# Performance work log

Measured on AMD Instinct MI355X. Metric: run time of the kernel, lower is better.

Reference implementation:

```python
import jax, jax.numpy as jnp
import numpy as np

B, S, T, H, E, V, PAD = 128, 400, 50, 512, 128, 50000, 1000


def setup_inputs() -> dict:
    key = jax.random.key(0)
    ks = jax.random.split(key, 20)
    inp = {
        "input_token": jax.random.randint(ks[0], (B, 1), 0, V),
        "prev_decoder_h_states": jax.random.normal(ks[1], (B, T, H), jnp.float32),
        "last_hidden": jax.random.normal(ks[2], (B, H), jnp.float32),
        "encoder_states": jax.random.normal(ks[3], (B, S, H), jnp.float32),
        "full_input_var": jax.random.randint(ks[4], (B, S), 0, V + PAD),
        "previous_att": jax.random.normal(ks[5], (B, T, S), jnp.float32),
        "control_var": jax.random.normal(ks[6], (B, 1), jnp.float32),
        # learned parameters
        "emb": jax.random.normal(ks[7], (V, E), jnp.float32) * 0.02,
        "W_ih": jax.random.normal(ks[8], (3 * H, E), jnp.float32) * 0.05,
        "W_hh": jax.random.normal(ks[9], (3 * H, H), jnp.float32) * 0.05,
        "b_ih": jnp.zeros((3 * H,), jnp.float32),
        "b_hh": jnp.zeros((3 * H,), jnp.float32),
        "w_h": jax.random.normal(ks[10], (H,), jnp.float32) * 0.05,
        "w_d": jax.random.normal(ks[11], (H,), jnp.float32) * 0.05,
        "gen_W": jax.random.normal(ks[12], (1, 3 * H + 1), jnp.float32) * 0.05,
        "gen_b": jnp.zeros((1,), jnp.float32),
        "outh_W": jax.random.normal(ks[13], (E, 3 * H + 1), jnp.float32) * 0.05,
        "outh_b": jnp.zeros((E,), jnp.float32),
        "outv_W": jax.random.normal(ks[14], (V, E), jnp.float32) * 0.02,
        "outv_b": jnp.zeros((V,), jnp.float32),
    }
    return inp


def reference(input_token, prev_decoder_h_states, last_hidden, encoder_states,
              full_input_var, previous_att, control_var,
              emb, W_ih, W_hh, b_ih, b_hh, w_h, w_d,
              gen_W, gen_b, outh_W, outh_b, outv_W, outv_b):
    # embedding lookup (dropout = eval-mode identity); seq len is 1
    x = emb[input_token[:, 0]]                              # [B,E]
    # single GRU step (torch gate order: r, z, n)
    gx = x @ W_ih.T + b_ih                                  # [B,3H]
    gh = last_hidden @ W_hh.T + b_hh                        # [B,3H]
    r = jax.nn.sigmoid(gx[:, :H] + gh[:, :H])
    z = jax.nn.sigmoid(gx[:, H:2 * H] + gh[:, H:2 * H])
    n = jnp.tanh(gx[:, 2 * H:] + r * gh[:, 2 * H:])
    h = (1.0 - z) * n + z * last_hidden                     # decoder_hidden [B,H]

    # temporal encoder attention (previous_att is not None branch)
    att_scores = jnp.einsum("bh,bsh->bs", h, w_h[None, None, :] * encoder_states)
    temporal = jnp.exp(att_scores) / jnp.exp(previous_att).sum(1)   # [B,S]
    new_previous_att = jnp.concatenate([previous_att, att_scores[:, None, :]], axis=1)
    att_dist = temporal / temporal.sum(-1, keepdims=True)           # [B,S]

    # intra-decoder attention
    dec_scores = jnp.einsum("bh,bth->bt", h, w_d[None, None, :] * prev_decoder_h_states)
    dec_att = jax.nn.softmax(dec_scores, axis=-1)                   # [B,T]
    decoder_context = jnp.einsum("bt,bth->bh", dec_att, prev_decoder_h_states)

    encoder_context = jnp.einsum("bs,bsh->bh", att_dist, encoder_states)
    combined = jnp.concatenate([h, encoder_context, decoder_context, control_var], axis=-1)  # [B,3H+1]

    p_vocab = jax.nn.softmax((combined @ outh_W.T + outh_b) @ outv_W.T + outv_b, axis=-1)    # [B,V]
    p_gen = jax.nn.sigmoid(combined @ gen_W.T + gen_b)                                       # [B,1]

    # copy distribution via scatter-add over extended vocab V+PAD
    token_input_dist = jnp.zeros((input_token.shape[0], V + PAD), p_vocab.dtype)
    rows = jnp.arange(input_token.shape[0])[:, None]
    token_input_dist = token_input_dist.at[rows, full_input_var].add(att_dist)

    p_final = jnp.pad(p_vocab * p_gen, ((0, 0), (0, PAD))) + (1.0 - p_gen) * token_input_dist
    decoder_h_states = jnp.concatenate([prev_decoder_h_states, h[:, None, :]], axis=1)
    return (p_final, p_gen, p_vocab, att_dist, decoder_h_states, h, new_previous_att)
```

## Files before the change

### kernel.cpp

```cpp
#include <hip/hip_runtime.h>
#include <hip/hip_bf16.h>
#include <math.h>

constexpr int B = 128, S = 400, T = 50, H = 512, E = 128, V = 50000, PADV = 1000;
constexpr int NV = V + PADV;
constexpr int TH1 = 3 * H + 1;

constexpr int O_PFINAL = 0;
constexpr int O_PGEN   = O_PFINAL + B * NV;
constexpr int O_PVOCAB = O_PGEN + B;
constexpr int O_ATT    = O_PVOCAB + B * V;
constexpr int O_DHS    = O_ATT + B * S;
constexpr int O_H      = O_DHS + B * (T + 1) * H;
constexpr int O_NPA    = O_H + B * H;

constexpr int W_X    = 0;
constexpr int W_GX   = W_X + B * E;
constexpr int W_GH   = W_GX + B * 3 * H;
constexpr int W_HW   = W_GH + B * 3 * H;
constexpr int W_HD   = W_HW + B * H;
constexpr int W_SC   = W_HD + B * H;
constexpr int W_DEN  = W_SC + B * S;
constexpr int W_CMB  = W_DEN + B * S;
constexpr int W_LE   = W_CMB + B * TH1;
constexpr int W_RMAX = W_LE + B * E;
constexpr int W_RSUM = W_RMAX + B;
constexpr int W_PM   = W_RSUM + B;
constexpr int W_PS   = W_PM + B * 10;

__device__ __forceinline__ float wave_sum(float v) {
#pragma unroll
  for (int o = 32; o > 0; o >>= 1) v += __shfl_xor(v, o);
  return v;
}

__global__ void k_init(const int* __restrict__ tok, const float* __restrict__ emb,
                       const float* __restrict__ ctrl, float* __restrict__ ws) {
  int i = blockIdx.x * 256 + threadIdx.x;
  if (i < B * E) {
    int b = i >> 7, e = i & 127;
    ws[W_X + i] = emb[tok[b] * E + e];
  }
  if (i < B * H) {
    int b = i >> 9, h = i & 511;
    ws[W_CMB + b * TH1 + H + h] = 0.f;
  }
  if (i < B) ws[W_CMB + i * TH1 + 3 * H] = ctrl[i];
#pragma unroll
  for (int j = 0; j < 3; ++j) ws[W_GH + i + j * 65536] = 0.f;
}

__global__ __launch_bounds__(256) void k_grugemm(
    const float* __restrict__ x, const float* __restrict__ lh,
    const float* __restrict__ Wih, const float* __restrict__ Whh,
    float* __restrict__ ws) {
  __shared__ float As[32][132];
  __shared__ float Ws[32][36];
  const int tid = threadIdx.x;
  const int n0 = blockIdx.x * 32;
  const int y = blockIdx.y;
  const bool g0 = (y == 0);
  const float* A = g0 ? x : lh;
  const float* W = g0 ? Wih : Whh;
  const int K = g0 ? E : H;
  const int kbase = g0 ? 0 : (y - 1) * 128;
  const int tc = tid & 15;
  const int tr = tid >> 4;
  float acc[8][2] = {};
  for (int c = 0; c < 4; ++c) {
    const int k0 = kbase + c * 32;
    {
      int i = tid;
#pragma unroll
      for (int it = 0; it < 4; ++it, i += 256) {
        int b = i >> 3, k4 = i & 7;
        float4 v = *(const float4*)&A[b * K + k0 + k4 * 4];
        As[k4 * 4 + 0][b] = v.x; As[k4 * 4 + 1][b] = v.y;
        As[k4 * 4 + 2][b] = v.z; As[k4 * 4 + 3][b] = v.w;
      }
    }
    {
      int n = tid >> 3, k4 = tid & 7;
      float4 v = *(const float4*)&W[(n0 + n) * K + k0 + k4 * 4];
      Ws[k4 * 4 + 0][n] = v.x; Ws[k4 * 4 + 1][n] = v.y;
      Ws[k4 * 4 + 2][n] = v.z; Ws[k4 * 4 + 3][n] = v.w;
    }
    __syncthreads();
#pragma unroll
    for (int kk = 0; kk < 32; ++kk) {
      float4 a0 = *(const float4*)&As[kk][tr * 8];
      float4 a1 = *(const float4*)&As[kk][tr * 8 + 4];
      float2 w = *(const float2*)&Ws[kk][tc * 2];
      float av[8] = {a0.x, a0.y, a0.z, a0.w, a1.x, a1.y, a1.z, a1.w};
#pragma unroll
      for (int i = 0; i < 8; ++i) {
        acc[i][0] += av[i] * w.x;
        acc[i][1] += av[i] * w.y;
      }
    }
    __syncthreads();
  }
  if (g0) {
#pragma unroll
    for (int i = 0; i < 8; ++i) {
      float* dst = ws + W_GX + (tr * 8 + i) * (3 * H) + n0 + tc * 2;
      dst[0] = acc[i][0]; dst[1] = acc[i][1];
    }
  } else {
#pragma unroll
    for (int i = 0; i < 8; ++i) {
      float* dst = ws + W_GH + (tr * 8 + i) * (3 * H) + n0 + tc * 2;
      atomicAdd(dst, acc[i][0]); atomicAdd(dst + 1, acc[i][1]);
    }
  }
}

__global__ void k_gates(const float* __restrict__ ws_in, const float* __restrict__ lh,
                        const float* __restrict__ bih, const float* __restrict__ bhh,
                        const float* __restrict__ w_h, const float* __restrict__ w_d,
                        float* __restrict__ ws, float* __restrict__ out) {
  int i = blockIdx.x * 256 + threadIdx.x;
  int b = i >> 9, u = i & 511;
  const float* gx = ws_in + W_GX + b * (3 * H);
  const float* gh = ws_in + W_GH + b * (3 * H);
  float gxr = gx[u] + bih[u], gxz = gx[H + u] + bih[H + u], gxn = gx[2 * H + u] + bih[2 * H + u];
  float ghr = gh[u] + bhh[u], ghz = gh[H + u] + bhh[H + u], ghn = gh[2 * H + u] + bhh[2 * H + u];
  float r = 1.f / (1.f + __expf(-(gxr + ghr)));
  float z = 1.f / (1.f + __expf(-(gxz + ghz)));
  float n = tanhf(gxn + r * ghn);
  float lhv = lh[i];
  float h = (1.f - z) * n + z * lhv;
  out[O_H + i] = h;
  out[O_DHS + b * ((T + 1) * H) + T * H + u] = h;
  ws[W_CMB + b * TH1 + u] = h;
  ws[W_HW + i] = h * w_h[u];
  ws[W_HD + i] = h * w_d[u];
}

__global__ void k_den(const float* __restrict__ pa, float* __restrict__ ws,
                      float* __restrict__ out) {
  int i = blockIdx.x * 256 + threadIdx.x;
  if (i >= B * S) return;
  int b = i / S, s = i - b * S;
  float acc = 0.f;
  for (int t = 0; t < T; ++t) {
    float v = pa[(b * T + t) * S + s];
    out[O_NPA + (b * (T + 1) + t) * S + s] = v;
    acc += __expf(v);
  }
  ws[W_DEN + i] = acc;
}

__global__ void k_escore(const float* __restrict__ enc, float* __restrict__ ws,
                         float* __restrict__ out) {
  int blk = blockIdx.x;
  int b = blk / 25, sgrp = blk % 25;
  int wave = threadIdx.x >> 6, lane = threadIdx.x & 63;
  const float4* hw4 = (const float4*)(ws + W_HW + b * H);
  float4 h0 = hw4[lane * 2], h1 = hw4[lane * 2 + 1];
#pragma unroll
  for (int ii = 0; ii < 4; ++ii) {
    int s = sgrp * 16 + wave * 4 + ii;
    const float4* e4 = (const float4*)(enc + (b * S + s) * H);
    float4 e0 = e4[lane * 2], e1 = e4[lane * 2 + 1];
    float d = h0.x * e0.x + h0.y * e0.y + h0.z * e0.z + h0.w * e0.w +
              h1.x * e1.x + h1.y * e1.y + h1.z * e1.z + h1.w * e1.w;
    d = wave_sum(d);
    if (lane == 0) {
      ws[W_SC + b * S + s] = d;
      out[O_NPA + (b * (T + 1) + T) * S + s] = d;
    }
  }
}

__global__ void k_attdist(const float* __restrict__ ws, float* __restrict__ out) {
  int b = blockIdx.x, tid = threadIdx.x;
  __shared__ float red[4];
  int s0 = tid, s1 = tid + 256;
  float t0 = __expf(ws[W_SC + b * S + s0]) / ws[W_DEN + b * S + s0];
  float t1 = 0.f;
  if (s1 < S) t1 = __expf(ws[W_SC + b * S + s1]) / ws[W_DEN + b * S + s1];
  float loc = wave_sum(t0 + t1);
  if ((tid & 63) == 0) red[tid >> 6] = loc;
  __syncthreads();
  float inv = 1.f / (red[0] + red[1] + red[2] + red[3]);
  out[O_ATT + b * S + s0] = t0 * inv;
  if (s1 < S) out[O_ATT + b * S + s1] = t1 * inv;
}

__global__ void k_dec(const float* __restrict__ pd, float* __restrict__ ws,
                      float* __restrict__ out) {
  int b = blockIdx.x, tid = threadIdx.x;
  int wave = tid >> 6, lane = tid & 63;
  __shared__ float sc[T];
  const float4* hd4 = (const float4*)(ws + W_HD + b * H);
  float4 d0 = hd4[lane * 2], d1 = hd4[lane * 2 + 1];
  for (int t = wave; t < T; t += 4) {
    const float4* p4 = (const float4*)(pd + (b * T + t) * H);
    float4 p0 = p4[lane * 2], p1 = p4[lane * 2 + 1];
    float v = d0.x * p0.x + d0.y * p0.y + d0.z * p0.z + d0.w * p0.w +
              d1.x * p1.x + d1.y * p1.y + d1.z * p1.z + d1.w * p1.w;
    v = wave_sum(v);
    if (lane == 0) sc[t] = v;
  }
  __syncthreads();
  if (tid < 64) {
    float v = (lane < T) ? sc[lane] : -1e30f;
    float m = v;
#pragma unroll
    for (int o = 32; o > 0; o >>= 1) m = fmaxf(m, __shfl_xor(m, o));
    float e = (lane < T) ? __expf(v - m) : 0.f;
    float ssum = wave_sum(e);
    if (lane < T) sc[lane] = e / ssum;
  }
  __syncthreads();
  float a0 = 0.f, a1 = 0.f;
  int h0 = tid, h1 = tid + 256;
  for (int t = 0; t < T; ++t) {
    float wt = sc[t];
    a0 += wt * pd[(b * T + t) * H + h0];
    a1 += wt * pd[(b * T + t) * H + h1];
  }
  ws[W_CMB + b * TH1 + 2 * H + h0] = a0;
  ws[W_CMB + b * TH1 + 2 * H + h1] = a1;
  const float4* src = (const float4*)(pd + b * T * H);
  float4* dst = (float4*)(out + O_DHS + b * (T + 1) * H);
  for (int i = tid; i < T * H / 4; i += 256) dst[i] = src[i];
}

__global__ void k_encctx(const float* __restrict__ enc, const float* __restrict__ out,
                         float* __restrict__ ws) {
  int blk = blockIdx.x;
  int b = blk / 5, c = blk % 5;
  int s0 = c * 80, tid = threadIdx.x;
  __shared__ float ad[80];
  if (tid < 80) ad[tid] = out[O_ATT + b * S + s0 + tid];
  __syncthreads();
  float a0 = 0.f, a1 = 0.f;
  int h0 = tid, h1 = tid + 256;
  for (int j = 0; j < 80; ++j) {
    float w = ad[j];
    const float* ep = enc + (b * S + s0 + j) * H;
    a0 += w * ep[h0];
    a1 += w * ep[h1];
  }
  atomicAdd(&ws[W_CMB + b * TH1 + H + h0], a0);
  atomicAdd(&ws[W_CMB + b * TH1 + H + h1], a1);
}

__global__ __launch_bounds__(256) void k_outh2(const float* __restrict__ oW,
                                               const float* __restrict__ ob,
                                               float* __restrict__ ws) {
  __shared__ float cmb[8 * TH1];
  const int tid = threadIdx.x;
  const int b0 = blockIdx.y * 8;
  const int e = blockIdx.x * 4 + (tid >> 6);
  const int lane = tid & 63;
  const float* src = ws + W_CMB + b0 * TH1;
  for (int i = tid; i < 8 * TH1; i += 256) cmb[i] = src[i];
  float wr[25];
  const float* wrow = oW + e * TH1;
#pragma unroll
  for (int j = 0; j < 25; ++j) {
    int k = lane + 64 * j;
    wr[j] = (k < TH1) ? wrow[k] : 0.f;
  }
  __syncthreads();
  float bias = ob[e];
#pragma unroll 1
  for (int bb = 0; bb < 8; ++bb) {
    const float* c = cmb + bb * TH1;
    float a = 0.f;
#pragma unroll
    for (int j = 0; j < 25; ++j) {
      int k = lane + 64 * j;
      float cv = (k < TH1) ? c[k] : 0.f;
      a += wr[j] * cv;
    }
    a = wave_sum(a);
    if (lane == 0) ws[W_LE + (b0 + bb) * E + e] = a + bias;
  }
}

__global__ void k_gen(const float* __restrict__ gW, const float* __restrict__ gb,
                      const float* __restrict__ ws, float* __restrict__ out) {
  int b = blockIdx.x, lane = threadIdx.x;
  float acc = 0.f;
  for (int k = lane; k < TH1; k += 64) acc += gW[k] * ws[W_CMB + b * TH1 + k];
  acc = wave_sum(acc);
  if (lane == 0) out[O_PGEN + b] = 1.f / (1.f + __expf(-(acc + gb[0])));
}

template <int BM, int BN, int BK, int TM, int TN>
__global__ __launch_bounds__(256) void gemm_abt(
    const float* __restrict__ A, const float* __restrict__ Bm,
    const float* __restrict__ bias, float* __restrict__ C, int M, int N, int K) {
  __shared__ float As[BK][BM + 4];
  __shared__ float Bs[BK][BN + 4];
  const int tid = threadIdx.x;
  const int m0 = blockIdx.y * BM, n0 = blockIdx.x * BN;
  constexpr int TC = BN / TN;
  const int tr = tid / TC, tc = tid % TC;
  float acc[TM][TN] = {};
  for (int k0 = 0; k0 < K; k0 += BK) {
    for (int i = tid; i < BM * BK; i += 256) {
      int m = i / BK, k = i % BK;
      float v = 0.f;
      if (m0 + m < M && k0 + k < K) v = A[(m0 + m) * K + k0 + k];
      As[k][m] = v;
    }
    for (int i = tid; i < BN * BK; i += 256) {
      int n = i / BK, k = i % BK;
      float v = 0.f;
      if (n0 + n < N && k0 + k < K) v = Bm[(n0 + n) * K + k0 + k];
      Bs[k][n] = v;
    }
    __syncthreads();
#pragma unroll
    for (int k = 0; k < BK; ++k) {
      float a[TM], bb[TN];
#pragma unroll
      for (int i = 0; i < TM; ++i) a[i] = As[k][tr * TM + i];
#pragma unroll
      for (int j = 0; j < TN; ++j) bb[j] = Bs[k][tc * TN + j];
#pragma unroll
      for (int i = 0; i < TM; ++i)
#pragma unroll
        for (int j = 0; j < TN; ++j) acc[i][j] += a[i] * bb[j];
    }
    __syncthreads();
  }
#pragma unroll
  for (int i = 0; i < TM; ++i) {
    int m = m0 + tr * TM + i;
    if (m >= M) continue;
#pragma unroll
    for (int j = 0; j < TN; ++j) {
      int n = n0 + tc * TN + j;
      if (n < N) C[m * N + n] = acc[i][j] + bias[n];
    }
  }
}

__global__ void k_rowstat1(const float* __restrict__ out, float* __restrict__ ws) {
  int c = blockIdx.x, b = blockIdx.y, tid = threadIdx.x;
  const float4* l4 = (const float4*)(out + O_PVOCAB + b * V);
  int base = c * 1250;
  float m = -1e30f, ssum = 0.f;
  for (int i = base + tid; i < base + 1250; i += 256) {
    float4 v = l4[i];
    float mm = fmaxf(fmaxf(v.x, v.y), fmaxf(v.z, v.w));
    if (mm > m) { ssum *= __expf(m - mm); m = mm; }
    ssum += __expf(v.x - m) + __expf(v.y - m) + __expf(v.z - m) + __expf(v.w - m);
  }
  __shared__ float mred[4], sred[4];
#pragma unroll
  for (int o = 32; o > 0; o >>= 1) {
    float om = __shfl_xor(m, o), os = __shfl_xor(ssum, o);
    float nm = fmaxf(m, om);
    ssum = ssum * __expf(m - nm) + os * __expf(om - nm);
    m = nm;
  }
  if ((tid & 63) == 0) { mred[tid >> 6] = m; sred[tid >> 6] = ssum; }
  __syncthreads();
  if (tid == 0) {
    float M = mred[0], SS = sred[0];
    for (int w = 1; w < 4; ++w) {
      float nm = fmaxf(M, mred[w]);
      SS = SS * __expf(M - nm) + sred[w] * __expf(mred[w] - nm);
      M = nm;
    }
    ws[W_PM + b * 10 + c] = M;
    ws[W_PS + b * 10 + c] = SS;
  }
}

__global__ void k_rowstat2(float* __restrict__ ws) {
  int b = threadIdx.x;
  float M = -1e30f;
#pragma unroll
  for (int c = 0; c < 10; ++c) M = fmaxf(M, ws[W_PM + b * 10 + c]);
  float SS = 0.f;
#pragma unroll
  for (int c = 0; c < 10; ++c) SS += ws[W_PS + b * 10 + c] * __expf(ws[W_PM + b * 10 + c] - M);
  ws[W_RMAX + b] = M;
  ws[W_RSUM + b] = SS;
}

__global__ void k_pvocab(const float* __restrict__ ws, float* __restrict__ out) {
  int b = blockIdx.y;
  int i = blockIdx.x * 256 + threadIdx.x;
  if (i >= V / 4) return;
  float m = ws[W_RMAX + b], inv = 1.f / ws[W_RSUM + b];
  float pg = out[O_PGEN + b];
  float4 v = ((const float4*)(out + O_PVOCAB + b * V))[i];
  float4 p;
  p.x = __expf(v.x - m) * inv;
  p.y = __expf(v.y - m) * inv;
  p.z = __expf(v.z - m) * inv;
  p.w = __expf(v.w - m) * inv;
  ((float4*)(out + O_PVOCAB + b * V))[i] = p;
  float4 pf;
  pf.x = pg * p.x; pf.y = pg * p.y; pf.z = pg * p.z; pf.w = pg * p.w;
  ((float4*)(out + O_PFINAL + b * NV))[i] = pf;
}

__global__ void k_pad(float* __restrict__ out) {
  int i = blockIdx.x * 256 + threadIdx.x;
  if (i >= B * PADV / 4) return;
  int b = i / (PADV / 4), j = i % (PADV / 4);
  ((float4*)(out + O_PFINAL + b * NV + V))[j] = make_float4(0.f, 0.f, 0.f, 0.f);
}

__global__ void k_scatter(const int* __restrict__ fiv, float* __restrict__ out) {
  int i = blockIdx.x * 256 + threadIdx.x;
  if (i >= B * S) return;
  int b = i / S;
  int idx = fiv[i];
  float pg = out[O_PGEN + b];
  float val = (1.f - pg) * out[O_ATT + i];
  atomicAdd(out + O_PFINAL + b * NV + idx, val);
}

extern "C" void kernel_launch(void* const* d_in, const int* in_sizes, int n_in,
                              void* d_out, int out_size, void* d_ws, size_t ws_size,
                              hipStream_t stream) {
  const int*   tok  = (const int*)d_in[0];
  const float* pd   = (const float*)d_in[1];
  const float* lh   = (const float*)d_in[2];
  const float* enc  = (const float*)d_in[3];
  const int*   fiv  = (const int*)d_in[4];
  const float* pa   = (const float*)d_in[5];
  const float* ctrl = (const float*)d_in[6];
  const float* emb  = (const float*)d_in[7];
  const float* W_ih = (const float*)d_in[8];
  const float* W_hh = (const float*)d_in[9];
  const float* b_ih = (const float*)d_in[10];
  const float* b_hh = (const float*)d_in[11];
  const float* w_h  = (const float*)d_in[12];
  const float* w_d  = (const float*)d_in[13];
  const float* gW   = (const float*)d_in[14];
  const float* gb   = (const float*)d_in[15];
  const float* ohW  = (const float*)d_in[16];
  const float* ohb  = (const float*)d_in[17];
  const float* ovW  = (const float*)d_in[18];
  const float* ovb  = (const float*)d_in[19];
  float* out = (float*)d_out;
  float* ws  = (float*)d_ws;

  k_init<<<256, 256, 0, stream>>>(tok, emb, ctrl, ws);
  k_grugemm<<<dim3(48, 5), 256, 0, stream>>>(ws + W_X, lh, W_ih, W_hh, ws);
  k_gates<<<256, 256, 0, stream>>>(ws, lh, b_ih, b_hh, w_h, w_d, ws, out);
  k_den<<<200, 256, 0, stream>>>(pa, ws, out);
  k_escore<<<3200, 256, 0, stream>>>(enc, ws, out);
  k_attdist<<<128, 256, 0, stream>>>(ws, out);
  k_dec<<<128, 256, 0, stream>>>(pd, ws, out);
  k_encctx<<<640, 256, 0, stream>>>(enc, out, ws);
  k_outh2<<<dim3(32, 16), 256, 0, stream>>>(ohW, ohb, ws);
  k_gen<<<128, 64, 0, stream>>>(gW, gb, ws, out);
  gemm_abt<128, 64, 32, 8, 4><<<dim3((V + 63) / 64, 1), 256, 0, stream>>>(ws + W_LE, ovW, ovb, out + O_PVOCAB, B, V, E);
  k_rowstat1<<<dim3(10, 128), 256, 0, stream>>>(out, ws);
  k_rowstat2<<<1, 128, 0, stream>>>(ws);
  k_pvocab<<<dim3(49, 128), 256, 0, stream>>>(ws, out);
  k_pad<<<125, 256, 0, stream>>>(out);
  k_scatter<<<200, 256, 0, stream>>>(fiv, out);
}
```

Before: 415.7 us.

## Fuse vocab GEMM with partial softmax stats and split out decoder-state copy

Replaces the generic vocab GEMM with a specialized 128x128-tile kernel that uses float4 loads and computes per-block row max and sum-exp in its epilogue. This removes the separate first row-stat pass that re-read the whole logits array. The second-stage reduction now works over 391 partials per row and runs as one block per row. The decoder-state copy moves out of the serial per-batch k_dec kernel into its own wide, fully parallel copy kernel. The cost is fewer GEMM blocks (391), with more registers per thread for the 8x8 accumulators.

```diff
diff --git a/kernel.cpp b/kernel.cpp
--- a/kernel.cpp
+++ b/kernel.cpp
@@ -5,6 +5,7 @@
 constexpr int B = 128, S = 400, T = 50, H = 512, E = 128, V = 50000, PADV = 1000;
 constexpr int NV = V + PADV;
 constexpr int TH1 = 3 * H + 1;
+constexpr int NBLK = 391;
 
 constexpr int O_PFINAL = 0;
 constexpr int O_PGEN   = O_PFINAL + B * NV;
@@ -26,7 +27,7 @@
 constexpr int W_RMAX = W_LE + B * E;
 constexpr int W_RSUM = W_RMAX + B;
 constexpr int W_PM   = W_RSUM + B;
-constexpr int W_PS   = W_PM + B * 10;
+constexpr int W_PS   = W_PM + B * NBLK;
 
 __device__ __forceinline__ float wave_sum(float v) {
 #pragma unroll
@@ -223,9 +224,13 @@
   }
   ws[W_CMB + b * TH1 + 2 * H + h0] = a0;
   ws[W_CMB + b * TH1 + 2 * H + h1] = a1;
-  const float4* src = (const float4*)(pd + b * T * H);
-  float4* dst = (float4*)(out + O_DHS + b * (T + 1) * H);
-  for (int i = tid; i < T * H / 4; i += 256) dst[i] = src[i];
+}
+
+__global__ void k_dhscopy(const float* __restrict__ pd, float* __restrict__ out) {
+  int i = blockIdx.x * 256 + threadIdx.x;
+  if (i >= B * T * H / 4) return;
+  int b = i / (T * H / 4), rem = i - b * (T * H / 4);
+  ((float4*)(out + O_DHS + b * (T + 1) * H))[rem] = ((const float4*)(pd + b * T * H))[rem];
 }
 
 __global__ void k_encctx(const float* __restrict__ enc, const float* __restrict__ out,
@@ -291,100 +296,115 @@
   if (lane == 0) out[O_PGEN + b] = 1.f / (1.f + __expf(-(acc + gb[0])));
 }
 
-template <int BM, int BN, int BK, int TM, int TN>
-__global__ __launch_bounds__(256) void gemm_abt(
-    const float* __restrict__ A, const float* __restrict__ Bm,
-    const float* __restrict__ bias, float* __restrict__ C, int M, int N, int K) {
-  __shared__ float As[BK][BM + 4];
-  __shared__ float Bs[BK][BN + 4];
+__global__ __launch_bounds__(256) void k_vgemm(
+    const float* __restrict__ A, const float* __restrict__ W,
+    const float* __restrict__ bias, float* __restrict__ C,
+    float* __restrict__ ws) {
+  __shared__ float As[32][132];
+  __shared__ float Bs[32][132];
   const int tid = threadIdx.x;
-  const int m0 = blockIdx.y * BM, n0 = blockIdx.x * BN;
-  constexpr int TC = BN / TN;
-  const int tr = tid / TC, tc = tid % TC;
-  float acc[TM][TN] = {};
-  for (int k0 = 0; k0 < K; k0 += BK) {
-    for (int i = tid; i < BM * BK; i += 256) {
-      int m = i / BK, k = i % BK;
-      float v = 0.f;
-      if (m0 + m < M && k0 + k < K) v = A[(m0 + m) * K + k0 + k];
-      As[k][m] = v;
-    }
-    for (int i = tid; i < BN * BK; i += 256) {
-      int n = i / BK, k = i % BK;
-      float v = 0.f;
-      if (n0 + n < N && k0 + k < K) v = Bm[(n0 + n) * K + k0 + k];
-      Bs[k][n] = v;
+  const int n0 = blockIdx.x * 128;
+  const int tr = tid >> 4;
+  const int tc = tid & 15;
+  float acc[8][8] = {};
+#pragma unroll 1
+  for (int c = 0; c < 4; ++c) {
+    const int k0 = c * 32;
+    {
+      int i = tid;
+#pragma unroll
+      for (int it = 0; it < 4; ++it, i += 256) {
+        int m = i >> 3, k4 = i & 7;
+        float4 v = *(const float4*)&A[m * 128 + k0 + k4 * 4];
+        As[k4 * 4 + 0][m] = v.x; As[k4 * 4 + 1][m] = v.y;
+        As[k4 * 4 + 2][m] = v.z; As[k4 * 4 + 3][m] = v.w;
+      }
+    }
+    {
+      int i = tid;
+#pragma unroll
+      for (int it = 0; it < 4; ++it, i += 256) {
+        int n = i >> 3, k4 = i & 7;
+        float4 v = make_float4(0.f, 0.f, 0.f, 0.f);
+        if (n0 + n < V) v = *(const float4*)&W[(n0 + n) * 128 + k0 + k4 * 4];
+        Bs[k4 * 4 + 0][n] = v.x; Bs[k4 * 4 + 1][n] = v.y;
+        Bs[k4 * 4 + 2][n] = v.z; Bs[k4 * 4 + 3][n] = v.w;
+      }
     }
     __syncthreads();
-#pragma unroll
-    for (int k = 0; k < BK; ++k) {
-      float a[TM], bb[TN];
-#pragma unroll
-      for (int i = 0; i < TM; ++i) a[i] = As[k][tr * TM + i];
-#pragma unroll
-      for (int j = 0; j < TN; ++j) bb[j] = Bs[k][tc * TN + j];
-#pragma unroll
-      for (int i = 0; i < TM; ++i)
-#pragma unroll
-        for (int j = 0; j < TN; ++j) acc[i][j] += a[i] * bb[j];
+#pragma unroll 4
+    for (int kk = 0; kk < 32; ++kk) {
+      float4 a0 = *(const float4*)&As[kk][tr * 8];
+      float4 a1 = *(const float4*)&As[kk][tr * 8 + 4];
+      float4 b0 = *(const float4*)&Bs[kk][tc * 8];
+      float4 b1 = *(const float4*)&Bs[kk][tc * 8 + 4];
+      float av[8] = {a0.x, a0.y, a0.z, a0.w, a1.x, a1.y, a1.z, a1.w};
+      float bw[8] = {b0.x, b0.y, b0.z, b0.w, b1.x, b1.y, b1.z, b1.w};
+#pragma unroll
+      for (int i = 0; i < 8; ++i)
+#pragma unroll
+        for (int j = 0; j < 8; ++j) acc[i][j] += av[i] * bw[j];
     }
     __syncthreads();
   }
-#pragma unroll
-  for (int i = 0; i < TM; ++i) {
-    int m = m0 + tr * TM + i;
-    if (m >= M) continue;
-#pragma unroll
-    for (int j = 0; j < TN; ++j) {
-      int n = n0 + tc * TN + j;
-      if (n < N) C[m * N + n] = acc[i][j] + bias[n];
-    }
-  }
-}
-
-__global__ void k_rowstat1(const float* __restrict__ out, float* __restrict__ ws) {
-  int c = blockIdx.x, b = blockIdx.y, tid = threadIdx.x;
-  const float4* l4 = (const float4*)(out + O_PVOCAB + b * V);
-  int base = c * 1250;
-  float m = -1e30f, ssum = 0.f;
-  for (int i = base + tid; i < base + 1250; i += 256) {
-    float4 v = l4[i];
-    float mm = fmaxf(fmaxf(v.x, v.y), fmaxf(v.z, v.w));
-    if (mm > m) { ssum *= __expf(m - mm); m = mm; }
-    ssum += __expf(v.x - m) + __expf(v.y - m) + __expf(v.z - m) + __expf(v.w - m);
-  }
-  __shared__ float mred[4], sred[4];
-#pragma unroll
-  for (int o = 32; o > 0; o >>= 1) {
-    float om = __shfl_xor(m, o), os = __shfl_xor(ssum, o);
-    float nm = fmaxf(m, om);
-    ssum = ssum * __expf(m - nm) + os * __expf(om - nm);
-    m = nm;
-  }
-  if ((tid & 63) == 0) { mred[tid >> 6] = m; sred[tid >> 6] = ssum; }
+  const int cbase = n0 + tc * 8;
+  float bv[8];
+#pragma unroll
+  for (int j = 0; j < 8; ++j) bv[j] = (cbase + j < V) ? bias[cbase + j] : 0.f;
+#pragma unroll
+  for (int i = 0; i < 8; ++i) {
+    int r = tr * 8 + i;
+    float m = -1e30f;
+#pragma unroll
+    for (int j = 0; j < 8; ++j) {
+      acc[i][j] += bv[j];
+      if (cbase + j < V) m = fmaxf(m, acc[i][j]);
+    }
+#pragma unroll
+    for (int o = 1; o < 16; o <<= 1) m = fmaxf(m, __shfl_xor(m, o));
+    float s = 0.f;
+#pragma unroll
+    for (int j = 0; j < 8; ++j)
+      if (cbase + j < V) s += __expf(acc[i][j] - m);
+#pragma unroll
+    for (int o = 1; o < 16; o <<= 1) s += __shfl_xor(s, o);
+    if (tc == 0) {
+      ws[W_PM + r * NBLK + blockIdx.x] = m;
+      ws[W_PS + r * NBLK + blockIdx.x] = s;
+    }
+    if (cbase + 8 <= V) {
+      *(float4*)&C[r * V + cbase] = make_float4(acc[i][0], acc[i][1], acc[i][2], acc[i][3]);
+      *(float4*)&C[r * V + cbase + 4] = make_float4(acc[i][4], acc[i][5], acc[i][6], acc[i][7]);
+    } else {
+#pragma unroll
+      for (int j = 0; j < 8; ++j)
+        if (cbase + j < V) C[r * V + cbase + j] = acc[i][j];
+    }
+  }
+}
+
+__global__ void k_rowstat2(float* __restrict__ ws) {
+  int b = blockIdx.x, tid = threadIdx.x;
+  const float* pm = ws + W_PM + b * NBLK;
+  const float* psv = ws + W_PS + b * NBLK;
+  __shared__ float red[4];
+  float m = -1e30f;
+  for (int c = tid; c < NBLK; c += 256) m = fmaxf(m, pm[c]);
+#pragma unroll
+  for (int o = 32; o > 0; o >>= 1) m = fmaxf(m, __shfl_xor(m, o));
+  if ((tid & 63) == 0) red[tid >> 6] = m;
+  __syncthreads();
+  float M = fmaxf(fmaxf(red[0], red[1]), fmaxf(red[2], red[3]));
+  __syncthreads();
+  float s = 0.f;
+  for (int c = tid; c < NBLK; c += 256) s += psv[c] * __expf(pm[c] - M);
+  s = wave_sum(s);
+  if ((tid & 63) == 0) red[tid >> 6] = s;
   __syncthreads();
   if (tid == 0) {
-    float M = mred[0], SS = sred[0];
-    for (int w = 1; w < 4; ++w) {
-      float nm = fmaxf(M, mred[w]);
-      SS = SS * __expf(M - nm) + sred[w] * __expf(mred[w] - nm);
-      M = nm;
-    }
-    ws[W_PM + b * 10 + c] = M;
-    ws[W_PS + b * 10 + c] = SS;
-  }
-}
-
-__global__ void k_rowstat2(float* __restrict__ ws) {
-  int b = threadIdx.x;
-  float M = -1e30f;
-#pragma unroll
-  for (int c = 0; c < 10; ++c) M = fmaxf(M, ws[W_PM + b * 10 + c]);
-  float SS = 0.f;
-#pragma unroll
-  for (int c = 0; c < 10; ++c) SS += ws[W_PS + b * 10 + c] * __expf(ws[W_PM + b * 10 + c] - M);
-  ws[W_RMAX + b] = M;
-  ws[W_RSUM + b] = SS;
+    ws[W_RMAX + b] = M;
+    ws[W_RSUM + b] = red[0] + red[1] + red[2] + red[3];
+  }
 }
 
 __global__ void k_pvocab(const float* __restrict__ ws, float* __restrict__ out) {
@@ -455,12 +475,12 @@
   k_escore<<<3200, 256, 0, stream>>>(enc, ws, out);
   k_attdist<<<128, 256, 0, stream>>>(ws, out);
   k_dec<<<128, 256, 0, stream>>>(pd, ws, out);
+  k_dhscopy<<<3200, 256, 0, stream>>>(pd, out);
   k_encctx<<<640, 256, 0, stream>>>(enc, out, ws);
   k_outh2<<<dim3(32, 16), 256, 0, stream>>>(ohW, ohb, ws);
   k_gen<<<128, 64, 0, stream>>>(gW, gb, ws, out);
-  gemm_abt<128, 64, 32, 8, 4><<<dim3((V + 63) / 64, 1), 256, 0, stream>>>(ws + W_LE, ovW, ovb, out + O_PVOCAB, B, V, E);
-  k_rowstat1<<<dim3(10, 128), 256, 0, stream>>>(out, ws);
-  k_rowstat2<<<1, 128, 0, stream>>>(ws);
+  k_vgemm<<<NBLK, 256, 0, stream>>>(ws + W_LE, ovW, ovb, out + O_PVOCAB, ws);
+  k_rowstat2<<<128, 256, 0, stream>>>(ws);
   k_pvocab<<<dim3(49, 128), 256, 0, stream>>>(ws, out);
   k_pad<<<125, 256, 0, stream>>>(out);
   k_scatter<<<200, 256, 0, stream>>>(fiv, out);
```

After: 386.7 us. 1.08x faster.
